# Optimization experiments

Hardware: AMD Instinct MI355X
Metric: run time of the kernel (lower is better)

Reference implementation:

```python
import jax, jax.numpy as jnp
import numpy as np

B, N, D_IN, D_OUT, L, T = 8, 512, 1024, 1024, 16, 4096


def setup_inputs() -> dict:
    key = jax.random.key(0)
    k1, k2, k3 = jax.random.split(key, 3)
    pooled_vectors = jax.random.normal(k1, (B, N, D_IN), dtype=jnp.float32)
    # stacked nn.Linear weights, each (out, in), bias=False
    W = jax.random.normal(k2, (L, D_OUT, D_IN), dtype=jnp.float32) * 0.02
    pooling_indices = jnp.sort(jax.random.randint(k3, (N,), 0, T, dtype=jnp.int64))
    return {
        "pooled_vectors": pooled_vectors,
        "W": W,
        "pooling_indices": pooling_indices,
        "target_length": T,
    }


def reference(pooled_vectors, W, pooling_indices, target_length):
    # pooled_vectors: (B, N, D_in); W: (L, D_out, D_in); pooling_indices: (N,) sorted
    Bn, Nn, _ = pooled_vectors.shape
    Ln = W.shape[0]
    t = jnp.arange(target_length)
    # segment i covers [start_i, idx_i + 1); searchsorted finds the covering segment
    seg = jnp.searchsorted(pooling_indices, t, side="left")  # (T,)
    valid = seg < Nn  # positions past the last pooling index stay zero
    segc = jnp.clip(seg, 0, Nn - 1)
    start = jnp.where(segc > 0, pooling_indices[segc - 1] + 1, 0)
    lidx = jnp.minimum(t - start, Ln - 1)  # position-specific linear index, capped
    # apply all L position linears to every pooled vector: (B, N, L, D_out)
    trans = jnp.einsum("bnd,lod->bnlo", pooled_vectors, W)
    out = trans[:, segc, lidx]  # gather per output position -> (B, T, D_out)
    return jnp.where(valid[None, :, None], out, jnp.zeros((), out.dtype))
```

## Files before the change

### kernel.cpp

```cpp
#include <hip/hip_runtime.h>
#include <stdint.h>

#define B_    8
#define N_    512
#define DIN   1024
#define DOUT  1024
#define L_    16
#define T_    4096

#define BM 256
#define BN 128
#define BK 32
#define NB (DOUT / BN)
#define NKT (DIN / BK)
#define MT_MAX 160
#define ZROW ((long)B_ * N_)

typedef __attribute__((ext_vector_type(8))) short short8;
typedef __attribute__((ext_vector_type(4))) float f32x4;

#define POOLED_ELEMS ((long)B_ * N_ * DIN + DIN)
#define WS_W_OFF     ((size_t)POOLED_ELEMS * 2)
#define WS_META_OFF  (WS_W_OFF + (size_t)L_ * DOUT * DIN * 2)

__device__ __forceinline__ unsigned short f2bf(float f) {
  unsigned u = __float_as_uint(f);
  u += 0x7FFFu + ((u >> 16) & 1u);
  return (unsigned short)(u >> 16);
}

__device__ __forceinline__ void gload_lds16(const void* g, void* l) {
  __builtin_amdgcn_global_load_lds(
      (const __attribute__((address_space(1))) void*)g,
      (__attribute__((address_space(3))) void*)l, 16, 0, 0);
}

__device__ __forceinline__ void bar() {
  asm volatile("" ::: "memory");
  __builtin_amdgcn_s_barrier();
  asm volatile("" ::: "memory");
}

__global__ void k_convert(const float* __restrict__ pooled,
                          const float* __restrict__ W,
                          unsigned short* __restrict__ wsP,
                          unsigned short* __restrict__ wsW) {
  const long np4 = (long)B_ * N_ * DIN / 4;
  const long nw4 = (long)L_ * DOUT * DIN / 4;
  const long nz4 = DIN / 4;
  long i = (long)blockIdx.x * blockDim.x + threadIdx.x;
  const long stride = (long)gridDim.x * blockDim.x;
  for (; i < np4 + nw4 + nz4; i += stride) {
    if (i < np4) {
      float4 v = ((const float4*)pooled)[i];
      ushort4 o = { f2bf(v.x), f2bf(v.y), f2bf(v.z), f2bf(v.w) };
      ((ushort4*)wsP)[i] = o;
    } else if (i < np4 + nw4) {
      float4 v = ((const float4*)W)[i - np4];
      ushort4 o = { f2bf(v.x), f2bf(v.y), f2bf(v.z), f2bf(v.w) };
      ((ushort4*)wsW)[i - np4] = o;
    } else {
      ushort4 z = {0, 0, 0, 0};
      ((ushort4*)wsP)[i - nw4] = z;
    }
  }
}

__global__ void k_prep(const int* __restrict__ pidx,
                       unsigned* __restrict__ tlist,
                       int* __restrict__ goff, int* __restrict__ grows,
                       unsigned* __restrict__ table, int* __restrict__ ntiles) {
  __shared__ int sp[N_];
  __shared__ int cnt[L_], pos[L_];
  const int tid = threadIdx.x;
  if (tid < N_) sp[tid] = pidx[tid];
  if (tid < L_) cnt[tid] = 0;
  __syncthreads();

  int start = tid ? sp[tid - 1] + 1 : 0;
  int len = sp[tid] - start + 1;
  if (len < 0) len = 0;
  const int nfull = len < 15 ? len : 15;

  for (int l2 = 0; l2 < nfull; ++l2) atomicAdd(&cnt[l2], 1);
  if (len > 15) atomicAdd(&cnt[15], (len - 15 + 254) / 255);
  if (tid == N_ - 1) {
    int invlen = T_ - 1 - sp[N_ - 1];
    if (invlen > 0) atomicAdd(&cnt[15], (invlen + 254) / 255);
  }
  __syncthreads();
  if (tid == 0) {
    int off = 0;
    for (int l2 = 0; l2 < L_; ++l2) {
      pos[l2] = off; goff[l2] = off; grows[l2] = cnt[l2] * B_;
      off += cnt[l2];
    }
  }
  __syncthreads();

  for (int l2 = 0; l2 < nfull; ++l2) {
    int p = atomicAdd(&pos[l2], 1);
    tlist[p] = (unsigned)(start + l2) | ((unsigned)tid << 12) | (1u << 22);
  }
  if (len > 15) {
    int rem = len - 15, tt2 = start + 15;
    while (rem > 0) {
      int rr = rem > 255 ? 255 : rem;
      int p = atomicAdd(&pos[15], 1);
      tlist[p] = (unsigned)tt2 | ((unsigned)tid << 12) | ((unsigned)rr << 22);
      tt2 += rr; rem -= rr;
    }
  }
  if (tid == N_ - 1) {
    int tt2 = sp[N_ - 1] + 1;
    int rem = T_ - tt2;
    while (rem > 0) {
      int rr = rem > 255 ? 255 : rem;
      int p = atomicAdd(&pos[15], 1);
      tlist[p] = (unsigned)tt2 | (1023u << 12) | ((unsigned)rr << 22);
      tt2 += rr; rem -= rr;
    }
  }
  __syncthreads();
  if (tid == 0) {
    int tt = 0;
    for (int l2 = 0; l2 < L_; ++l2) {
      int rows = cnt[l2] * B_;
      for (int r0 = 0; r0 < rows; r0 += BM) table[tt++] = (unsigned)l2 | ((unsigned)r0 << 4);
    }
    *ntiles = tt;
  }
}

__global__ __launch_bounds__(512, 4)
void k_gemm(const unsigned short* __restrict__ wsP,
            const unsigned short* __restrict__ wsW,
            const unsigned* __restrict__ tlist,
            const int* __restrict__ goff,
            const int* __restrict__ grows,
            const unsigned* __restrict__ table,
            const int* __restrict__ ntiles,
            float* __restrict__ out) {
  const int bid = blockIdx.x;
  const int mt = bid >> 3;
  const int nt = bid & 7;
  if (mt >= *ntiles) return;

  const unsigned te = table[mt];
  const int l    = te & 15;
  const int row0 = (int)(te >> 4);
  const int toff = goff[l];
  const int rows = grows[l];

  __shared__ __align__(16) unsigned short As[3][BM * BK];
  __shared__ __align__(16) unsigned short Bs[3][BN * BK];

  const int tid  = threadIdx.x;
  const int lane = tid & 63;
  const int w    = tid >> 6;
  const int wm   = w >> 1;
  const int wn   = w & 1;

  const int srow = tid >> 2;
  const int sx4  = ((tid & 3) ^ ((srow >> 1) & 3)) * 16;
  const char* aptr0;
  const char* aptr1;
  {
    long re[2];
#pragma unroll
    for (int r = 0; r < 2; ++r) {
      int rg = row0 + r * 128 + srow;
      if (rg < rows) {
        unsigned e = tlist[toff + (rg >> 3)];
        unsigned n = (e >> 12) & 0x3FF;
        int b = rg & 7;
        re[r] = (n >= N_) ? ZROW * (long)DIN
                          : ((long)(b * N_ + (int)n)) * DIN;
      } else re[r] = ZROW * (long)DIN;
    }
    aptr0 = (const char*)(wsP + re[0]) + sx4;
    aptr1 = (const char*)(wsP + re[1]) + sx4;
  }
  const char* bptr = (const char*)(wsW + ((long)l * DOUT + nt * BN + srow) * DIN) + sx4;

#define STG(t_, sb) do { \
  gload_lds16(aptr0 + (t_) * 64, (char*)As[sb] + w * 1024); \
  gload_lds16(aptr1 + (t_) * 64, (char*)As[sb] + 8192 + w * 1024); \
  gload_lds16(bptr  + (t_) * 64, (char*)Bs[sb] + w * 1024); } while (0)

  const int arow = wm * 64 + (lane & 15);
  const int brow = wn * 64 + (lane & 15);
  const int axr  = ((lane >> 4) ^ (((lane & 15) >> 1) & 3)) * 16;

  f32x4 acc[4][4];
#pragma unroll
  for (int m = 0; m < 4; ++m)
#pragma unroll
    for (int n = 0; n < 4; ++n)
      acc[m][n] = (f32x4){0.f, 0.f, 0.f, 0.f};

  short8 af[4], bf[4];

#define PHASE(t_, bb, sb) do { \
  const int t2_ = (t_) + 2; \
  if (t2_ < NKT) STG(t2_, sb); \
  _Pragma("unroll") for (int m_ = 0; m_ < 4; ++m_) \
    af[m_] = *(const short8*)((const char*)As[bb] + (arow + m_ * 16) * 64 + axr); \
  _Pragma("unroll") for (int n_ = 0; n_ < 4; ++n_) \
    bf[n_] = *(const short8*)((const char*)Bs[bb] + (brow + n_ * 16) * 64 + axr); \
  bar(); \
  asm volatile("s_waitcnt lgkmcnt(0)" ::: "memory"); \
  __builtin_amdgcn_s_setprio(1); \
  _Pragma("unroll") for (int n_ = 0; n_ < 4; ++n_) \
    _Pragma("unroll") for (int m_ = 0; m_ < 4; ++m_) \
      acc[m_][n_] = __builtin_amdgcn_mfma_f32_16x16x32_bf16(af[m_], bf[n_], acc[m_][n_], 0, 0, 0); \
  __builtin_amdgcn_s_setprio(0); \
  if (t2_ < NKT) asm volatile("s_waitcnt vmcnt(3)" ::: "memory"); \
  else           asm volatile("s_waitcnt vmcnt(0)" ::: "memory"); \
  bar(); \
} while (0)

  STG(0, 0);
  STG(1, 1);
  asm volatile("s_waitcnt vmcnt(3)" ::: "memory");
  bar();

  for (int j = 0; j < 11; ++j) {
    const int t0 = 3 * j;
    if (t0     < NKT) PHASE(t0,     0, 2);
    if (t0 + 1 < NKT) PHASE(t0 + 1, 1, 0);
    if (t0 + 2 < NKT) PHASE(t0 + 2, 2, 1);
  }

#pragma unroll
  for (int m = 0; m < 4; ++m) {
#pragma unroll
    for (int jj = 0; jj < 4; ++jj) {
      int rt = wm * 64 + m * 16 + (lane >> 4) * 4 + jj;
      int rg = row0 + rt;
      if (rg >= rows) continue;
      unsigned e = tlist[toff + (rg >> 3)];
      int b = rg & 7;
      int t0 = (int)(e & 0xFFFu);
      int rep = (int)(e >> 22);
      float* orow = out + ((long)b * T_ + t0) * DOUT + nt * BN + wn * 64 + (lane & 15);
      for (int r = 0; r < rep; ++r) {
#pragma unroll
        for (int n = 0; n < 4; ++n)
          orow[n * 16] = acc[m][n][jj];
        orow += DOUT;
      }
    }
  }
#undef STG
#undef PHASE
}

extern "C" void kernel_launch(void* const* d_in, const int* in_sizes, int n_in,
                              void* d_out, int out_size, void* d_ws, size_t ws_size,
                              hipStream_t stream) {
  const float* pooled = (const float*)d_in[0];
  const float* W      = (const float*)d_in[1];
  const int*   pidx   = (const int*)d_in[2];
  float* out = (float*)d_out;

  char* ws = (char*)d_ws;
  unsigned short* wsP = (unsigned short*)(ws);
  unsigned short* wsW = (unsigned short*)(ws + WS_W_OFF);
  int* meta  = (int*)(ws + WS_META_OFF);
  unsigned* tlist = (unsigned*)meta;
  int* goff  = meta + 8 * T_;
  int* grows = meta + 8 * T_ + 16;
  unsigned* table = (unsigned*)(meta + 8 * T_ + 32);
  int* ntiles = meta + 8 * T_ + 32 + MT_MAX;

  k_prep<<<1, 512, 0, stream>>>(pidx, tlist, goff, grows, table, ntiles);
  k_convert<<<2048, 256, 0, stream>>>(pooled, W, wsP, wsW);
  k_gemm<<<MT_MAX * NB, 512, 0, stream>>>(wsP, wsW, tlist, goff, grows, table,
                                          ntiles, out);
}
```

Before: 137.8 us.

## Replace LDS-staged GEMM with per-wave register-direct 64x64 tiles

Removes the shared-memory triple-buffered pipeline with global_load_lds and barriers. Each wave now independently computes a 64x64 output tile, loading A and B fragments straight from global memory into registers with a two-stage register double buffer. The goal is to drop barrier and LDS overhead and to get finer-grained tiles for the ragged per-linear row groups. In exchange there is no data reuse across waves through LDS, so global and L2 traffic per FLOP rises, and the per-lane strided 16-byte loads are less coalesced.

After: 314.2 us. 128% more time.

```diff
diff --git a/kernel.cpp b/kernel.cpp
--- a/kernel.cpp
+++ b/kernel.cpp
@@ -8,12 +8,9 @@
 #define L_    16
 #define T_    4096
 
-#define BM 256
-#define BN 128
-#define BK 32
-#define NB (DOUT / BN)
-#define NKT (DIN / BK)
-#define MT_MAX 160
+#define WMR 64
+#define MT_PAD 544
+#define MB_PER_NT (MT_PAD / 4)
 #define ZROW ((long)B_ * N_)
 
 typedef __attribute__((ext_vector_type(8))) short short8;
@@ -27,18 +24,6 @@
   unsigned u = __float_as_uint(f);
   u += 0x7FFFu + ((u >> 16) & 1u);
   return (unsigned short)(u >> 16);
-}
-
-__device__ __forceinline__ void gload_lds16(const void* g, void* l) {
-  __builtin_amdgcn_global_load_lds(
-      (const __attribute__((address_space(1))) void*)g,
-      (__attribute__((address_space(3))) void*)l, 16, 0, 0);
-}
-
-__device__ __forceinline__ void bar() {
-  asm volatile("" ::: "memory");
-  __builtin_amdgcn_s_barrier();
-  asm volatile("" ::: "memory");
 }
 
 __global__ void k_convert(const float* __restrict__ pooled,
@@ -126,13 +111,13 @@
     int tt = 0;
     for (int l2 = 0; l2 < L_; ++l2) {
       int rows = cnt[l2] * B_;
-      for (int r0 = 0; r0 < rows; r0 += BM) table[tt++] = (unsigned)l2 | ((unsigned)r0 << 4);
+      for (int r0 = 0; r0 < rows; r0 += WMR) table[tt++] = (unsigned)l2 | ((unsigned)r0 << 4);
     }
     *ntiles = tt;
   }
 }
 
-__global__ __launch_bounds__(512, 4)
+__global__ __launch_bounds__(256, 2)
 void k_gemm(const unsigned short* __restrict__ wsP,
             const unsigned short* __restrict__ wsW,
             const unsigned* __restrict__ tlist,
@@ -141,56 +126,39 @@
             const unsigned* __restrict__ table,
             const int* __restrict__ ntiles,
             float* __restrict__ out) {
-  const int bid = blockIdx.x;
-  const int mt = bid >> 3;
-  const int nt = bid & 7;
-  if (mt >= *ntiles) return;
-
-  const unsigned te = table[mt];
+  const int w     = threadIdx.x >> 6;
+  const int lane  = threadIdx.x & 63;
+  const int ntile = blockIdx.x / MB_PER_NT;
+  const int mtile = (blockIdx.x % MB_PER_NT) * 4 + w;
+  if (mtile >= *ntiles) return;
+
+  const unsigned te = table[mtile];
   const int l    = te & 15;
   const int row0 = (int)(te >> 4);
   const int toff = goff[l];
   const int rows = grows[l];
 
-  __shared__ __align__(16) unsigned short As[3][BM * BK];
-  __shared__ __align__(16) unsigned short Bs[3][BN * BK];
-
-  const int tid  = threadIdx.x;
-  const int lane = tid & 63;
-  const int w    = tid >> 6;
-  const int wm   = w >> 1;
-  const int wn   = w & 1;
-
-  const int srow = tid >> 2;
-  const int sx4  = ((tid & 3) ^ ((srow >> 1) & 3)) * 16;
-  const char* aptr0;
-  const char* aptr1;
-  {
-    long re[2];
-#pragma unroll
-    for (int r = 0; r < 2; ++r) {
-      int rg = row0 + r * 128 + srow;
-      if (rg < rows) {
-        unsigned e = tlist[toff + (rg >> 3)];
-        unsigned n = (e >> 12) & 0x3FF;
-        int b = rg & 7;
-        re[r] = (n >= N_) ? ZROW * (long)DIN
+  const int lr = lane & 15;
+  const int kh = lane >> 4;
+
+  const unsigned short* pa[4];
+#pragma unroll
+  for (int m = 0; m < 4; ++m) {
+    int rg = row0 + m * 16 + lr;
+    long rowElem;
+    if (rg < rows) {
+      unsigned e = tlist[toff + (rg >> 3)];
+      unsigned n = (e >> 12) & 0x3FF;
+      int b = rg & 7;
+      rowElem = (n >= N_) ? ZROW * (long)DIN
                           : ((long)(b * N_ + (int)n)) * DIN;
-      } else re[r] = ZROW * (long)DIN;
-    }
-    aptr0 = (const char*)(wsP + re[0]) + sx4;
-    aptr1 = (const char*)(wsP + re[1]) + sx4;
-  }
-  const char* bptr = (const char*)(wsW + ((long)l * DOUT + nt * BN + srow) * DIN) + sx4;
-
-#define STG(t_, sb) do { \
-  gload_lds16(aptr0 + (t_) * 64, (char*)As[sb] + w * 1024); \
-  gload_lds16(aptr1 + (t_) * 64, (char*)As[sb] + 8192 + w * 1024); \
-  gload_lds16(bptr  + (t_) * 64, (char*)Bs[sb] + w * 1024); } while (0)
-
-  const int arow = wm * 64 + (lane & 15);
-  const int brow = wn * 64 + (lane & 15);
-  const int axr  = ((lane >> 4) ^ (((lane & 15) >> 1) & 3)) * 16;
+    } else rowElem = ZROW * (long)DIN;
+    pa[m] = wsP + rowElem + kh * 8;
+  }
+  const unsigned short* pb[4];
+#pragma unroll
+  for (int n = 0; n < 4; ++n)
+    pb[n] = wsW + ((long)l * DOUT + ntile * 64 + n * 16 + lr) * DIN + kh * 8;
 
   f32x4 acc[4][4];
 #pragma unroll
@@ -199,51 +167,55 @@
     for (int n = 0; n < 4; ++n)
       acc[m][n] = (f32x4){0.f, 0.f, 0.f, 0.f};
 
-  short8 af[4], bf[4];
-
-#define PHASE(t_, bb, sb) do { \
-  const int t2_ = (t_) + 2; \
-  if (t2_ < NKT) STG(t2_, sb); \
-  _Pragma("unroll") for (int m_ = 0; m_ < 4; ++m_) \
-    af[m_] = *(const short8*)((const char*)As[bb] + (arow + m_ * 16) * 64 + axr); \
-  _Pragma("unroll") for (int n_ = 0; n_ < 4; ++n_) \
-    bf[n_] = *(const short8*)((const char*)Bs[bb] + (brow + n_ * 16) * 64 + axr); \
-  bar(); \
-  asm volatile("s_waitcnt lgkmcnt(0)" ::: "memory"); \
-  __builtin_amdgcn_s_setprio(1); \
-  _Pragma("unroll") for (int n_ = 0; n_ < 4; ++n_) \
-    _Pragma("unroll") for (int m_ = 0; m_ < 4; ++m_) \
-      acc[m_][n_] = __builtin_amdgcn_mfma_f32_16x16x32_bf16(af[m_], bf[n_], acc[m_][n_], 0, 0, 0); \
-  __builtin_amdgcn_s_setprio(0); \
-  if (t2_ < NKT) asm volatile("s_waitcnt vmcnt(3)" ::: "memory"); \
-  else           asm volatile("s_waitcnt vmcnt(0)" ::: "memory"); \
-  bar(); \
-} while (0)
-
-  STG(0, 0);
-  STG(1, 1);
-  asm volatile("s_waitcnt vmcnt(3)" ::: "memory");
-  bar();
-
-  for (int j = 0; j < 11; ++j) {
-    const int t0 = 3 * j;
-    if (t0     < NKT) PHASE(t0,     0, 2);
-    if (t0 + 1 < NKT) PHASE(t0 + 1, 1, 0);
-    if (t0 + 2 < NKT) PHASE(t0 + 2, 2, 1);
-  }
-
+  short8 a0[4], b0[4], a1[4], b1[4];
 #pragma unroll
   for (int m = 0; m < 4; ++m) {
+    a0[m] = *(const short8*)(pa[m]);
+    a1[m] = *(const short8*)(pa[m] + 32);
+  }
+#pragma unroll
+  for (int n = 0; n < 4; ++n) {
+    b0[n] = *(const short8*)(pb[n]);
+    b1[n] = *(const short8*)(pb[n] + 32);
+  }
+
+#pragma unroll
+  for (int s = 0; s < 32; s += 2) {
+#pragma unroll
+    for (int n = 0; n < 4; ++n)
+#pragma unroll
+      for (int m = 0; m < 4; ++m)
+        acc[m][n] = __builtin_amdgcn_mfma_f32_16x16x32_bf16(a0[m], b0[n], acc[m][n], 0, 0, 0);
+    if (s + 2 < 32) {
+#pragma unroll
+      for (int m = 0; m < 4; ++m) a0[m] = *(const short8*)(pa[m] + (s + 2) * 32);
+#pragma unroll
+      for (int n = 0; n < 4; ++n) b0[n] = *(const short8*)(pb[n] + (s + 2) * 32);
+    }
+#pragma unroll
+    for (int n = 0; n < 4; ++n)
+#pragma unroll
+      for (int m = 0; m < 4; ++m)
+        acc[m][n] = __builtin_amdgcn_mfma_f32_16x16x32_bf16(a1[m], b1[n], acc[m][n], 0, 0, 0);
+    if (s + 3 < 32) {
+#pragma unroll
+      for (int m = 0; m < 4; ++m) a1[m] = *(const short8*)(pa[m] + (s + 3) * 32);
+#pragma unroll
+      for (int n = 0; n < 4; ++n) b1[n] = *(const short8*)(pb[n] + (s + 3) * 32);
+    }
+  }
+
+#pragma unroll
+  for (int m = 0; m < 4; ++m) {
 #pragma unroll
     for (int jj = 0; jj < 4; ++jj) {
-      int rt = wm * 64 + m * 16 + (lane >> 4) * 4 + jj;
-      int rg = row0 + rt;
+      int rg = row0 + m * 16 + (lane >> 4) * 4 + jj;
       if (rg >= rows) continue;
       unsigned e = tlist[toff + (rg >> 3)];
       int b = rg & 7;
       int t0 = (int)(e & 0xFFFu);
       int rep = (int)(e >> 22);
-      float* orow = out + ((long)b * T_ + t0) * DOUT + nt * BN + wn * 64 + (lane & 15);
+      float* orow = out + ((long)b * T_ + t0) * DOUT + ntile * 64 + lr;
       for (int r = 0; r < rep; ++r) {
 #pragma unroll
         for (int n = 0; n < 4; ++n)
@@ -252,8 +224,6 @@
       }
     }
   }
-#undef STG
-#undef PHASE
 }
 
 extern "C" void kernel_launch(void* const* d_in, const int* in_sizes, int n_in,
@@ -272,10 +242,10 @@
   int* goff  = meta + 8 * T_;
   int* grows = meta + 8 * T_ + 16;
   unsigned* table = (unsigned*)(meta + 8 * T_ + 32);
-  int* ntiles = meta + 8 * T_ + 32 + MT_MAX;
+  int* ntiles = meta + 8 * T_ + 32 + MT_PAD;
 
   k_prep<<<1, 512, 0, stream>>>(pidx, tlist, goff, grows, table, ntiles);
   k_convert<<<2048, 256, 0, stream>>>(pooled, W, wsP, wsW);
-  k_gemm<<<MT_MAX * NB, 512, 0, stream>>>(wsP, wsW, tlist, goff, grows, table,
-                                          ntiles, out);
-}
+  k_gemm<<<16 * MB_PER_NT, 256, 0, stream>>>(wsP, wsW, tlist, goff, grows,
+                                             table, ntiles, out);
+}
```
